# Optimization experiments

Hardware: AMD Instinct MI355X
Metric: run time of the kernel (lower is better)

## Reference

```python
import jax, jax.numpy as jnp
import numpy as np

N = 50000       # nodes
E = 800000      # directed edges (before self-loops)
IN = 128        # in_channels
H = 8           # heads
C = 32          # hidden_channels (per head)
OUT = 4         # out_channels
NS_ATT = 0.2    # PyG GATConv attention leaky-relu slope
NS_ACT = 0.01   # model activation leaky-relu slope
EPS = 1e-5      # BatchNorm eps


def setup_inputs() -> dict:
    key = jax.random.key(0)
    ks = jax.random.split(key, 18)
    s = 0.05
    return {
        "x": jax.random.normal(ks[0], (N, IN), jnp.float32),
        "edge_index": jax.random.randint(ks[1], (2, E), 0, N, dtype=jnp.int32),
        # layer 1: GATConv(IN -> C, heads=H, concat)
        "W1": jax.random.normal(ks[2], (IN, H * C), jnp.float32) * s,
        "as1": jax.random.normal(ks[3], (H, C), jnp.float32) * s,
        "ad1": jax.random.normal(ks[4], (H, C), jnp.float32) * s,
        "b1": jnp.zeros((H * C,), jnp.float32),
        "g1": jnp.ones((H * C,), jnp.float32),
        "be1": jnp.zeros((H * C,), jnp.float32),
        # middle layer: GATConv(H*C -> C, heads=H, concat) + BN + residual
        "W2": jax.random.normal(ks[5], (H * C, H * C), jnp.float32) * s,
        "as2": jax.random.normal(ks[6], (H, C), jnp.float32) * s,
        "ad2": jax.random.normal(ks[7], (H, C), jnp.float32) * s,
        "b2": jnp.zeros((H * C,), jnp.float32),
        "g2": jnp.ones((H * C,), jnp.float32),
        "be2": jnp.zeros((H * C,), jnp.float32),
        # final layer: GATConv(H*C -> OUT, heads=1, concat=False)
        "W3": jax.random.normal(ks[8], (H * C, OUT), jnp.float32) * s,
        "as3": jax.random.normal(ks[9], (1, OUT), jnp.float32) * s,
        "ad3": jax.random.normal(ks[10], (1, OUT), jnp.float32) * s,
        "b3": jnp.zeros((OUT,), jnp.float32),
    }


def _lrelu(x, slope):
    return jnp.where(x >= 0, x, slope * x)


def _gat_conv(x, src, dst, W, a_src, a_dst, bias, heads, ch, concat):
    # PyG GATConv: h = x @ W per head; edge logit = LReLU(a_src.h_j + a_dst.h_i)
    n = x.shape[0]
    h = (x @ W).reshape(n, heads, ch)                      # [N,H,C]
    al_s = jnp.sum(h * a_src, axis=-1)                     # [N,H]
    al_d = jnp.sum(h * a_dst, axis=-1)                     # [N,H]
    logits = _lrelu(al_s[src] + al_d[dst], NS_ATT)         # [E,H]
    # segment softmax over edges grouped by destination node
    m = jax.ops.segment_max(logits, dst, num_segments=n)   # [N,H]
    e = jnp.exp(logits - m[dst])
    denom = jax.ops.segment_sum(e, dst, num_segments=n)
    alpha = e / (denom[dst] + 1e-16)                       # [E,H]
    out = jax.ops.segment_sum(alpha[:, :, None] * h[src], dst, num_segments=n)  # [N,H,C]
    if concat:
        return out.reshape(n, heads * ch) + bias
    return out.mean(axis=1) + bias


def _bn(x, gamma, beta):
    mu = jnp.mean(x, axis=0)
    var = jnp.mean((x - mu) ** 2, axis=0)
    return (x - mu) * jax.lax.rsqrt(var + EPS) * gamma + beta


def reference(x, edge_index, W1, as1, ad1, b1, g1, be1,
              W2, as2, ad2, b2, g2, be2, W3, as3, ad3, b3):
    n = x.shape[0]
    loops = jnp.arange(n, dtype=edge_index.dtype)          # self-loops (PyG default)
    src = jnp.concatenate([edge_index[0], loops])
    dst = jnp.concatenate([edge_index[1], loops])
    h = _lrelu(_bn(_gat_conv(x, src, dst, W1, as1, ad1, b1, H, C, True), g1, be1), NS_ACT)
    residual = h
    h = _lrelu(_bn(_gat_conv(h, src, dst, W2, as2, ad2, b2, H, C, True), g2, be2), NS_ACT)
    h = h + residual
    return _gat_conv(h, src, dst, W3, as3, ad3, b3, 1, OUT, False)
```

## Files before the change

kernel.cpp:

```cpp
#include <hip/hip_runtime.h>

typedef __attribute__((ext_vector_type(8))) short bf16x8;
typedef __attribute__((ext_vector_type(4))) float f32x4;

__device__ __forceinline__ float lrelu(float x, float s) { return x >= 0.f ? x : s * x; }
__device__ __forceinline__ float b2f(unsigned short u) {
  union { unsigned int i; float f; } v; v.i = ((unsigned int)u) << 16; return v.f;
}
__device__ __forceinline__ float b2f_lo(unsigned int u) {
  union { unsigned int i; float f; } v; v.i = u << 16; return v.f;
}
__device__ __forceinline__ float b2f_hi(unsigned int u) {
  union { unsigned int i; float f; } v; v.i = u & 0xffff0000u; return v.f;
}
__device__ __forceinline__ unsigned short f2b(float f) {
  union { float f; unsigned int i; } v; v.f = f;
  unsigned int r = v.i + 0x7fffu + ((v.i >> 16) & 1u);
  return (unsigned short)(r >> 16);
}
__device__ __forceinline__ unsigned int fbits(float f) {
  union { float f; unsigned int i; } v; v.f = f; return v.i;
}
__device__ __forceinline__ float bitsf(unsigned int u) {
  union { unsigned int i; float f; } v; v.i = u; return v.f;
}

__global__ __launch_bounds__(256) void k_hist(const int* __restrict__ dst, int e,
                                              int* __restrict__ cnt) {
  int i = blockIdx.x * 256 + threadIdx.x;
  if (i < e) atomicAdd(&cnt[dst[i]], 1);
}

__global__ __launch_bounds__(256) void k_bsum(const int* __restrict__ cnt,
                                              int* __restrict__ bsum, int n) {
  const int base = blockIdx.x * 1024;
  const int t = threadIdx.x;
  int s = 0;
#pragma unroll
  for (int i = 0; i < 4; ++i) {
    int idx = base + t + i * 256;
    if (idx < n) s += cnt[idx] + 1;
  }
#pragma unroll
  for (int off = 1; off < 64; off <<= 1) s += __shfl_xor(s, off);
  __shared__ int ws[4];
  const int lane = t & 63, w = t >> 6;
  if (lane == 0) ws[w] = s;
  __syncthreads();
  if (t == 0) bsum[blockIdx.x] = ws[0] + ws[1] + ws[2] + ws[3];
}

__global__ __launch_bounds__(64) void k_scanb(const int* __restrict__ bsum,
                                              int* __restrict__ boff,
                                              int* __restrict__ ptrN, int B) {
  const int lane = threadIdx.x;
  int v = lane < B ? bsum[lane] : 0;
  int incl = v;
#pragma unroll
  for (int off = 1; off < 64; off <<= 1) {
    int u = __shfl_up(incl, off);
    if (lane >= off) incl += u;
  }
  if (lane < B) boff[lane] = incl - v;
  if (lane == 63) *ptrN = incl;
}

__global__ __launch_bounds__(256) void k_scanl(const int* __restrict__ cnt,
                                               const int* __restrict__ boff,
                                               int* __restrict__ ptr,
                                               int* __restrict__ fill, int n) {
  __shared__ int ws[4];
  const int t = threadIdx.x;
  const int base = blockIdx.x * 1024 + t * 4;
  int v0 = base + 0 < n ? cnt[base + 0] + 1 : 0;
  int v1 = base + 1 < n ? cnt[base + 1] + 1 : 0;
  int v2 = base + 2 < n ? cnt[base + 2] + 1 : 0;
  int v3 = base + 3 < n ? cnt[base + 3] + 1 : 0;
  const int tsum = v0 + v1 + v2 + v3;
  const int lane = t & 63, w = t >> 6;
  int incl = tsum;
#pragma unroll
  for (int off = 1; off < 64; off <<= 1) {
    int u = __shfl_up(incl, off);
    if (lane >= off) incl += u;
  }
  if (lane == 63) ws[w] = incl;
  __syncthreads();
  int excl = boff[blockIdx.x] + incl - tsum;
  for (int i = 0; i < w; ++i) excl += ws[i];
  if (base + 0 < n) { ptr[base + 0] = excl; fill[base + 0] = excl; }
  excl += v0;
  if (base + 1 < n) { ptr[base + 1] = excl; fill[base + 1] = excl; }
  excl += v1;
  if (base + 2 < n) { ptr[base + 2] = excl; fill[base + 2] = excl; }
  excl += v2;
  if (base + 3 < n) { ptr[base + 3] = excl; fill[base + 3] = excl; }
}

__global__ __launch_bounds__(256) void k_scatter(const int* __restrict__ srce,
                                                 const int* __restrict__ dste,
                                                 int e, int n,
                                                 int* __restrict__ fill,
                                                 int* __restrict__ srcs) {
  int i = blockIdx.x * 256 + threadIdx.x;
  if (i < e) {
    int pos = atomicAdd(&fill[dste[i]], 1);
    srcs[pos] = srce[i];
  } else if (i < e + n) {
    int v = i - e;
    int pos = atomicAdd(&fill[v], 1);
    srcs[pos] = v;
  }
}

__global__ __launch_bounds__(256) void k_prep(const float* __restrict__ x,
                                              unsigned short* __restrict__ xb,
                                              const float* __restrict__ W1,
                                              unsigned short* __restrict__ w1t,
                                              const float* __restrict__ W2,
                                              unsigned short* __restrict__ w2t, int n4) {
  int i = blockIdx.x * 256 + threadIdx.x;
  if (i < n4) {
    float4 v = ((const float4*)x)[i];
    ushort4 o;
    o.x = f2b(v.x); o.y = f2b(v.y); o.z = f2b(v.z); o.w = f2b(v.w);
    ((ushort4*)xb)[i] = o;
    return;
  }
  i -= n4;
  if (i < 256 * 128) {
    int nn = i / 128, k = i - nn * 128;
    w1t[i] = f2b(W1[(size_t)k * 256 + nn]);
    return;
  }
  i -= 256 * 128;
  if (i < 256 * 256) {
    int nn = i / 256, k = i - nn * 256;
    w2t[i] = f2b(W2[(size_t)k * 256 + nn]);
  }
}

__global__ __launch_bounds__(256) void k_mfma(const unsigned short* __restrict__ A,
                                              const unsigned short* __restrict__ BT,
                                              unsigned short* __restrict__ C,
                                              const float* __restrict__ as_,
                                              const float* __restrict__ ad_,
                                              float* __restrict__ als,
                                              float* __restrict__ ald,
                                              int M, int Nn, int K) {
  __shared__ unsigned int Asu[128 * 20];
  __shared__ unsigned int Bsu[128 * 20];
  const int tid = threadIdx.x;
  const int bm = blockIdx.x * 128, bn = blockIdx.y * 128;
  const int w = tid >> 6, lane = tid & 63;
  const int wm = w >> 1, wn = w & 1;
  const int l16 = lane & 15, lg = lane >> 4;
  f32x4 acc[4][4] = {};
  for (int k0 = 0; k0 < K; k0 += 32) {
#pragma unroll
    for (int rep = 0; rep < 2; ++rep) {
      int ci = tid + rep * 256;
      int row = ci >> 2, cg = ci & 3;
      int ar = bm + row;
      ar = ar < M ? ar : M - 1;
      uint4 av = *(const uint4*)(A + (size_t)ar * K + k0 + cg * 8);
      *(uint4*)&Asu[row * 20 + cg * 4] = av;
      uint4 bv = *(const uint4*)(BT + (size_t)(bn + row) * K + k0 + cg * 8);
      *(uint4*)&Bsu[row * 20 + cg * 4] = bv;
    }
    __syncthreads();
    bf16x8 aF[4], bF[4];
#pragma unroll
    for (int mi = 0; mi < 4; ++mi)
      aF[mi] = *(const bf16x8*)&Asu[(wm * 64 + mi * 16 + l16) * 20 + lg * 4];
#pragma unroll
    for (int ni = 0; ni < 4; ++ni)
      bF[ni] = *(const bf16x8*)&Bsu[(wn * 64 + ni * 16 + l16) * 20 + lg * 4];
#pragma unroll
    for (int mi = 0; mi < 4; ++mi)
#pragma unroll
      for (int ni = 0; ni < 4; ++ni)
        acc[mi][ni] =
            __builtin_amdgcn_mfma_f32_16x16x32_bf16(aF[mi], bF[ni], acc[mi][ni], 0, 0, 0);
    __syncthreads();
  }
  float asv[4], adv[4];
#pragma unroll
  for (int ni = 0; ni < 4; ++ni) {
    int gcol = bn + wn * 64 + ni * 16 + l16;
    asv[ni] = as_[gcol];
    adv[ni] = ad_[gcol];
  }
  const int hb = (bn >> 5) + wn * 2;
#pragma unroll
  for (int mi = 0; mi < 4; ++mi) {
#pragma unroll
    for (int r = 0; r < 4; ++r) {
      int grow = bm + wm * 64 + mi * 16 + lg * 4 + r;
      bool ok = grow < M;
      if (ok) {
#pragma unroll
        for (int ni = 0; ni < 4; ++ni) {
          int gcol = bn + wn * 64 + ni * 16 + l16;
          C[(size_t)grow * Nn + gcol] = f2b(acc[mi][ni][r]);
        }
      }
      float ps0 = acc[mi][0][r] * asv[0] + acc[mi][1][r] * asv[1];
      float ps1 = acc[mi][2][r] * asv[2] + acc[mi][3][r] * asv[3];
      float pd0 = acc[mi][0][r] * adv[0] + acc[mi][1][r] * adv[1];
      float pd1 = acc[mi][2][r] * adv[2] + acc[mi][3][r] * adv[3];
#pragma unroll
      for (int off = 1; off < 16; off <<= 1) {
        ps0 += __shfl_xor(ps0, off);
        ps1 += __shfl_xor(ps1, off);
        pd0 += __shfl_xor(pd0, off);
        pd1 += __shfl_xor(pd1, off);
      }
      if (ok && l16 == 0) {
        *(float2*)(als + (size_t)grow * 8 + hb) = make_float2(ps0, ps1);
        *(float2*)(ald + (size_t)grow * 8 + hb) = make_float2(pd0, pd1);
      }
    }
  }
}

__global__ __launch_bounds__(256) void k_agg(const unsigned short* __restrict__ h,
                                             const float* __restrict__ als,
                                             const float* __restrict__ ald,
                                             const int* __restrict__ ptr,
                                             const int* __restrict__ srcs,
                                             const float* __restrict__ bias,
                                             unsigned short* __restrict__ out, int n) {
  int wid = (blockIdx.x * 256 + threadIdx.x) >> 6;
  int lane = threadIdx.x & 63;
  if (wid >= n) return;
  const int beg = ptr[wid], end = ptr[wid + 1];
  const int L = lane & 15;
  const int e = lane >> 4;
  const int hh = L >> 1;
  const float adh = ald[(size_t)wid * 8 + hh];
  float s = 0.f;
  float a0 = 0, a1 = 0, a2 = 0, a3 = 0, a4 = 0, a5 = 0, a6 = 0, a7 = 0;
  float a8 = 0, a9 = 0, aA = 0, aB = 0, aC = 0, aD = 0, aE = 0, aF = 0;
  int j = beg + e;
  int s0 = j < end ? srcs[j] : 0;
  int s1 = (j + 4) < end ? srcs[j + 4] : 0;
  const uint4* hp0 = (const uint4*)(h + (size_t)s0 * 256 + L * 16);
  uint4 c0 = hp0[0];
  uint4 c1 = hp0[1];
  float alsc = als[(size_t)s0 * 8 + hh];
  for (; j < end; j += 4) {
    int s2 = (j + 8) < end ? srcs[j + 8] : 0;
    const uint4* hp1 = (const uint4*)(h + (size_t)s1 * 256 + L * 16);
    uint4 n0 = hp1[0];
    uint4 n1 = hp1[1];
    float alsn = als[(size_t)s1 * 8 + hh];
    float lg = lrelu(alsc + adh, 0.2f);
    float wt = __expf(lg);
    s += wt;
    a0 += wt * b2f_lo(c0.x); a1 += wt * b2f_hi(c0.x);
    a2 += wt * b2f_lo(c0.y); a3 += wt * b2f_hi(c0.y);
    a4 += wt * b2f_lo(c0.z); a5 += wt * b2f_hi(c0.z);
    a6 += wt * b2f_lo(c0.w); a7 += wt * b2f_hi(c0.w);
    a8 += wt * b2f_lo(c1.x); a9 += wt * b2f_hi(c1.x);
    aA += wt * b2f_lo(c1.y); aB += wt * b2f_hi(c1.y);
    aC += wt * b2f_lo(c1.z); aD += wt * b2f_hi(c1.z);
    aE += wt * b2f_lo(c1.w); aF += wt * b2f_hi(c1.w);
    c0 = n0; c1 = n1; alsc = alsn;
    s1 = s2;
  }
  a0 += __shfl_xor(a0, 16); a0 += __shfl_xor(a0, 32);
  a1 += __shfl_xor(a1, 16); a1 += __shfl_xor(a1, 32);
  a2 += __shfl_xor(a2, 16); a2 += __shfl_xor(a2, 32);
  a3 += __shfl_xor(a3, 16); a3 += __shfl_xor(a3, 32);
  a4 += __shfl_xor(a4, 16); a4 += __shfl_xor(a4, 32);
  a5 += __shfl_xor(a5, 16); a5 += __shfl_xor(a5, 32);
  a6 += __shfl_xor(a6, 16); a6 += __shfl_xor(a6, 32);
  a7 += __shfl_xor(a7, 16); a7 += __shfl_xor(a7, 32);
  a8 += __shfl_xor(a8, 16); a8 += __shfl_xor(a8, 32);
  a9 += __shfl_xor(a9, 16); a9 += __shfl_xor(a9, 32);
  aA += __shfl_xor(aA, 16); aA += __shfl_xor(aA, 32);
  aB += __shfl_xor(aB, 16); aB += __shfl_xor(aB, 32);
  aC += __shfl_xor(aC, 16); aC += __shfl_xor(aC, 32);
  aD += __shfl_xor(aD, 16); aD += __shfl_xor(aD, 32);
  aE += __shfl_xor(aE, 16); aE += __shfl_xor(aE, 32);
  aF += __shfl_xor(aF, 16); aF += __shfl_xor(aF, 32);
  s += __shfl_xor(s, 16); s += __shfl_xor(s, 32);
  const float inv = 1.f / (s + 1e-16f);
  if (e == 0) {
    const float4* bp = (const float4*)(bias + L * 16);
    float4 b0 = bp[0], b1 = bp[1], b2 = bp[2], b3 = bp[3];
    uint4 o0, o1;
    o0.x = (unsigned int)f2b(a0 * inv + b0.x) | ((unsigned int)f2b(a1 * inv + b0.y) << 16);
    o0.y = (unsigned int)f2b(a2 * inv + b0.z) | ((unsigned int)f2b(a3 * inv + b0.w) << 16);
    o0.z = (unsigned int)f2b(a4 * inv + b1.x) | ((unsigned int)f2b(a5 * inv + b1.y) << 16);
    o0.w = (unsigned int)f2b(a6 * inv + b1.z) | ((unsigned int)f2b(a7 * inv + b1.w) << 16);
    o1.x = (unsigned int)f2b(a8 * inv + b2.x) | ((unsigned int)f2b(a9 * inv + b2.y) << 16);
    o1.y = (unsigned int)f2b(aA * inv + b2.z) | ((unsigned int)f2b(aB * inv + b2.w) << 16);
    o1.z = (unsigned int)f2b(aC * inv + b3.x) | ((unsigned int)f2b(aD * inv + b3.y) << 16);
    o1.w = (unsigned int)f2b(aE * inv + b3.z) | ((unsigned int)f2b(aF * inv + b3.w) << 16);
    uint4* op = (uint4*)(out + (size_t)wid * 256 + L * 16);
    op[0] = o0;
    op[1] = o1;
  }
}

__global__ __launch_bounds__(256) void k_bnp1(const unsigned short* __restrict__ x,
                                              float* __restrict__ partial, int n) {
  const int t = threadIdx.x;
  const int q = t & 63;
  const int rsub = t >> 6;
  float s0 = 0, s1 = 0, s2 = 0, s3 = 0, q0 = 0, q1 = 0, q2 = 0, q3 = 0;
  int r = blockIdx.x * 4 + rsub;
  for (; r + 6144 < n; r += 8192) {
    ushort4 va = *(const ushort4*)(x + (size_t)r * 256 + q * 4);
    ushort4 vb = *(const ushort4*)(x + (size_t)(r + 2048) * 256 + q * 4);
    ushort4 vc = *(const ushort4*)(x + (size_t)(r + 4096) * 256 + q * 4);
    ushort4 vd = *(const ushort4*)(x + (size_t)(r + 6144) * 256 + q * 4);
    float f;
    f = b2f(va.x); s0 += f; q0 += f * f;
    f = b2f(va.y); s1 += f; q1 += f * f;
    f = b2f(va.z); s2 += f; q2 += f * f;
    f = b2f(va.w); s3 += f; q3 += f * f;
    f = b2f(vb.x); s0 += f; q0 += f * f;
    f = b2f(vb.y); s1 += f; q1 += f * f;
    f = b2f(vb.z); s2 += f; q2 += f * f;
    f = b2f(vb.w); s3 += f; q3 += f * f;
    f = b2f(vc.x); s0 += f; q0 += f * f;
    f = b2f(vc.y); s1 += f; q1 += f * f;
    f = b2f(vc.z); s2 += f; q2 += f * f;
    f = b2f(vc.w); s3 += f; q3 += f * f;
    f = b2f(vd.x); s0 += f; q0 += f * f;
    f = b2f(vd.y); s1 += f; q1 += f * f;
    f = b2f(vd.z); s2 += f; q2 += f * f;
    f = b2f(vd.w); s3 += f; q3 += f * f;
  }
  for (; r < n; r += 2048) {
    ushort4 v = *(const ushort4*)(x + (size_t)r * 256 + q * 4);
    float f;
    f = b2f(v.x); s0 += f; q0 += f * f;
    f = b2f(v.y); s1 += f; q1 += f * f;
    f = b2f(v.z); s2 += f; q2 += f * f;
    f = b2f(v.w); s3 += f; q3 += f * f;
  }
  __shared__ float ls[4][512];
  ls[rsub][q * 4 + 0] = s0; ls[rsub][q * 4 + 1] = s1;
  ls[rsub][q * 4 + 2] = s2; ls[rsub][q * 4 + 3] = s3;
  ls[rsub][256 + q * 4 + 0] = q0; ls[rsub][256 + q * 4 + 1] = q1;
  ls[rsub][256 + q * 4 + 2] = q2; ls[rsub][256 + q * 4 + 3] = q3;
  __syncthreads();
  float a = ls[0][t] + ls[1][t] + ls[2][t] + ls[3][t];
  float b = ls[0][256 + t] + ls[1][256 + t] + ls[2][256 + t] + ls[3][256 + t];
  partial[blockIdx.x * 512 + t] = a;
  partial[blockIdx.x * 512 + 256 + t] = b;
}

__global__ __launch_bounds__(256) void k_bnp2(const float* __restrict__ partial,
                                              const float* __restrict__ ga,
                                              const float* __restrict__ be,
                                              float* __restrict__ ss, float invn) {
  const int c = blockIdx.x * 4 + (threadIdx.x >> 6);
  const int lane = threadIdx.x & 63;
  float s = 0.f, qq = 0.f;
#pragma unroll
  for (int k = 0; k < 8; ++k) {
    int b = lane + k * 64;
    s += partial[(size_t)b * 512 + c];
    qq += partial[(size_t)b * 512 + 256 + c];
  }
#pragma unroll
  for (int off = 1; off < 64; off <<= 1) {
    s += __shfl_xor(s, off);
    qq += __shfl_xor(qq, off);
  }
  if (lane == 0) {
    float mu = s * invn;
    float var = qq * invn - mu * mu;
    float sc = ga[c] * rsqrtf(var + 1e-5f);
    ss[c] = sc;
    ss[256 + c] = be[c] - mu * sc;
  }
}

__global__ __launch_bounds__(256) void k_bnact(const unsigned short* __restrict__ x,
                                               const float* __restrict__ ss,
                                               unsigned short* __restrict__ out, int n) {
  const int tot4 = n * 64;
  for (int t = blockIdx.x * 256 + threadIdx.x; t < tot4; t += gridDim.x * 256) {
    int i0 = t * 4;
    int c = i0 & 255;
    ushort4 xu = *(const ushort4*)(x + i0);
    float4 scv = *(const float4*)(ss + c);
    float4 shv = *(const float4*)(ss + 256 + c);
    float t0 = b2f(xu.x) * scv.x + shv.x;
    float t1 = b2f(xu.y) * scv.y + shv.y;
    float t2 = b2f(xu.z) * scv.z + shv.z;
    float t3 = b2f(xu.w) * scv.w + shv.w;
    float o0 = fmaxf(t0, 0.01f * t0);
    float o1 = fmaxf(t1, 0.01f * t1);
    float o2 = fmaxf(t2, 0.01f * t2);
    float o3 = fmaxf(t3, 0.01f * t3);
    ushort4 ob;
    ob.x = f2b(o0); ob.y = f2b(o1); ob.z = f2b(o2); ob.w = f2b(o3);
    *(ushort4*)(out + i0) = ob;
  }
}

__global__ __launch_bounds__(256) void k_bnact3(const unsigned short* __restrict__ x,
                                                const float* __restrict__ ss,
                                                const unsigned short* __restrict__ res,
                                                const float* __restrict__ W3,
                                                const float* __restrict__ as3,
                                                const float* __restrict__ ad3,
                                                uint4* __restrict__ h3p, int n) {
  int wid = (blockIdx.x * 256 + threadIdx.x) >> 6;
  int lane = threadIdx.x & 63;
  if (wid >= n) return;
  const int c = lane * 4;
  ushort4 xu = *(const ushort4*)(x + (size_t)wid * 256 + c);
  ushort4 rv = *(const ushort4*)(res + (size_t)wid * 256 + c);
  float4 scv = *(const float4*)(ss + c);
  float4 shv = *(const float4*)(ss + 256 + c);
  float t0 = b2f(xu.x) * scv.x + shv.x;
  float t1 = b2f(xu.y) * scv.y + shv.y;
  float t2 = b2f(xu.z) * scv.z + shv.z;
  float t3 = b2f(xu.w) * scv.w + shv.w;
  float o0 = fmaxf(t0, 0.01f * t0) + b2f(rv.x);
  float o1 = fmaxf(t1, 0.01f * t1) + b2f(rv.y);
  float o2 = fmaxf(t2, 0.01f * t2) + b2f(rv.z);
  float o3 = fmaxf(t3, 0.01f * t3) + b2f(rv.w);
  const float4* Wp = (const float4*)W3 + lane * 4;
  float4 w0 = Wp[0], w1 = Wp[1], w2 = Wp[2], w3 = Wp[3];
  float a0 = o0 * w0.x + o1 * w1.x + o2 * w2.x + o3 * w3.x;
  float a1 = o0 * w0.y + o1 * w1.y + o2 * w2.y + o3 * w3.y;
  float a2 = o0 * w0.z + o1 * w1.z + o2 * w2.z + o3 * w3.z;
  float a3 = o0 * w0.w + o1 * w1.w + o2 * w2.w + o3 * w3.w;
#pragma unroll
  for (int off = 1; off < 64; off <<= 1) {
    a0 += __shfl_xor(a0, off);
    a1 += __shfl_xor(a1, off);
    a2 += __shfl_xor(a2, off);
    a3 += __shfl_xor(a3, off);
  }
  if (lane == 0) {
    float als3v = a0 * as3[0] + a1 * as3[1] + a2 * as3[2] + a3 * as3[3];
    float ald3v = a0 * ad3[0] + a1 * ad3[1] + a2 * ad3[2] + a3 * ad3[3];
    uint4 pv;
    pv.x = (unsigned int)f2b(a0) | ((unsigned int)f2b(a1) << 16);
    pv.y = (unsigned int)f2b(a2) | ((unsigned int)f2b(a3) << 16);
    pv.z = fbits(als3v);
    pv.w = fbits(ald3v);
    h3p[wid] = pv;
  }
}

__global__ __launch_bounds__(256) void k_agg3(const uint4* __restrict__ h3p,
                                              const int* __restrict__ ptr,
                                              const int* __restrict__ srcs,
                                              const float* __restrict__ b3,
                                              float* __restrict__ out, int n) {
  int wid = (blockIdx.x * 256 + threadIdx.x) >> 6;
  int lane = threadIdx.x & 63;
  if (wid >= n) return;
  const int beg = ptr[wid], end = ptr[wid + 1];
  const float aldh = bitsf(h3p[wid].w);
  float s = 0.f, a0 = 0.f, a1 = 0.f, a2 = 0.f, a3 = 0.f;
  for (int j = beg + lane; j < end; j += 64) {
    uint4 v = h3p[srcs[j]];
    float wgt = __expf(lrelu(bitsf(v.z) + aldh, 0.2f));
    s += wgt;
    a0 += wgt * b2f_lo(v.x);
    a1 += wgt * b2f_hi(v.x);
    a2 += wgt * b2f_lo(v.y);
    a3 += wgt * b2f_hi(v.y);
  }
#pragma unroll
  for (int off = 1; off < 64; off <<= 1) {
    s += __shfl_xor(s, off);
    a0 += __shfl_xor(a0, off);
    a1 += __shfl_xor(a1, off);
    a2 += __shfl_xor(a2, off);
    a3 += __shfl_xor(a3, off);
  }
  if (lane == 0) {
    float inv = 1.f / (s + 1e-16f);
    out[(size_t)wid * 4 + 0] = a0 * inv + b3[0];
    out[(size_t)wid * 4 + 1] = a1 * inv + b3[1];
    out[(size_t)wid * 4 + 2] = a2 * inv + b3[2];
    out[(size_t)wid * 4 + 3] = a3 * inv + b3[3];
  }
}

extern "C" void kernel_launch(void* const* d_in, const int* in_sizes, int n_in,
                              void* d_out, int out_size, void* d_ws, size_t ws_size,
                              hipStream_t stream) {
  const float* x   = (const float*)d_in[0];
  const int*   ei  = (const int*)d_in[1];
  const float* W1  = (const float*)d_in[2];
  const float* as1 = (const float*)d_in[3];
  const float* ad1 = (const float*)d_in[4];
  const float* b1  = (const float*)d_in[5];
  const float* ga1 = (const float*)d_in[6];
  const float* be1 = (const float*)d_in[7];
  const float* W2  = (const float*)d_in[8];
  const float* as2 = (const float*)d_in[9];
  const float* ad2 = (const float*)d_in[10];
  const float* b2  = (const float*)d_in[11];
  const float* ga2 = (const float*)d_in[12];
  const float* be2 = (const float*)d_in[13];
  const float* W3  = (const float*)d_in[14];
  const float* as3 = (const float*)d_in[15];
  const float* ad3 = (const float*)d_in[16];
  const float* b3  = (const float*)d_in[17];

  const int N = in_sizes[0] / 128;
  const int E = in_sizes[1] / 2;
  const int ET = E + N;
  float* out = (float*)d_out;

  char* w = (char*)d_ws;
  auto alloc = [&](size_t bytes) -> void* {
    void* p = (void*)w;
    w += (bytes + 255) & ~(size_t)255;
    return p;
  };
  int* ptr              = (int*)alloc((size_t)(N + 1) * 4);
  int* fill             = (int*)alloc((size_t)N * 4);
  int* cnt              = (int*)alloc((size_t)N * 4);
  int* bsum             = (int*)alloc(64 * 4);
  int* boff             = (int*)alloc(64 * 4);
  int* srcs             = (int*)alloc((size_t)ET * 4);
  unsigned short* hbuf  = (unsigned short*)alloc((size_t)N * 256 * 2);
  unsigned short* aggb  = (unsigned short*)alloc((size_t)N * 256 * 2);
  unsigned short* a1b   = (unsigned short*)alloc((size_t)N * 256 * 2);
  unsigned short* xb    = (unsigned short*)alloc((size_t)N * 128 * 2);
  unsigned short* w1t   = (unsigned short*)alloc(256 * 128 * 2);
  unsigned short* w2t   = (unsigned short*)alloc(256 * 256 * 2);
  float* als            = (float*)alloc((size_t)N * 8 * 4);
  float* ald            = (float*)alloc((size_t)N * 8 * 4);
  uint4* h3p            = (uint4*)alloc((size_t)N * 16);
  float* partial        = (float*)alloc(512 * 512 * 4);
  float* ss             = (float*)alloc(1024 * 4);

  const int* esrc = ei;
  const int* edst = ei + E;
  const float invn = 1.f / (float)N;

  hipMemsetAsync(cnt, 0, (size_t)N * 4, stream);

  const int B = (N + 1023) / 1024;
  k_hist<<<(E + 255) / 256, 256, 0, stream>>>(edst, E, cnt);
  k_bsum<<<B, 256, 0, stream>>>(cnt, bsum, N);
  k_scanb<<<1, 64, 0, stream>>>(bsum, boff, ptr + N, B);
  k_scanl<<<B, 256, 0, stream>>>(cnt, boff, ptr, fill, N);
  k_scatter<<<(ET + 255) / 256, 256, 0, stream>>>(esrc, edst, E, N, fill, srcs);

  const int n4 = N * 32;
  const int prep_tot = n4 + 256 * 128 + 256 * 256;
  k_prep<<<(prep_tot + 255) / 256, 256, 0, stream>>>(x, xb, W1, w1t, W2, w2t, n4);

  const dim3 gemm_grid((N + 127) / 128, 2);
  const int wblocks = (N + 3) / 4;

  k_mfma<<<gemm_grid, 256, 0, stream>>>(xb, w1t, hbuf, as1, ad1, als, ald, N, 256, 128);
  k_agg<<<wblocks, 256, 0, stream>>>(hbuf, als, ald, ptr, srcs, b1, aggb, N);
  k_bnp1<<<512, 256, 0, stream>>>(aggb, partial, N);
  k_bnp2<<<64, 256, 0, stream>>>(partial, ga1, be1, ss, invn);
  k_bnact<<<2048, 256, 0, stream>>>(aggb, ss, a1b, N);

  k_mfma<<<gemm_grid, 256, 0, stream>>>(a1b, w2t, hbuf, as2, ad2, als, ald, N, 256, 256);
  k_agg<<<wblocks, 256, 0, stream>>>(hbuf, als, ald, ptr, srcs, b2, aggb, N);
  k_bnp1<<<512, 256, 0, stream>>>(aggb, partial, N);
  k_bnp2<<<64, 256, 0, stream>>>(partial, ga2, be2, ss + 512, invn);
  k_bnact3<<<wblocks, 256, 0, stream>>>(aggb, ss + 512, a1b, W3, as3, ad3, h3p, N);

  k_agg3<<<wblocks, 256, 0, stream>>>(h3p, ptr, srcs, b3, out, N);
}
```

Baseline: 376.5 us.

## Trim launches, fold memset into prep, and use 16-lane groups in final aggregation

The separate block-offset scan kernel is removed: each scanl block now scans the block sums itself. The memset of the count array moves into the prep kernel, which now runs first. The final single-head aggregation gives each node 16 lanes instead of a full 64-lane wavefront, with a vectorized float4 output store. The scatter writes use nontemporal stores. Together these cut launch count and idle lanes, at the cost of redundant per-block scans and less parallelism for high-degree nodes.

```diff
diff --git a/kernel.cpp b/kernel.cpp
--- a/kernel.cpp
+++ b/kernel.cpp
@@ -50,27 +50,24 @@
   if (t == 0) bsum[blockIdx.x] = ws[0] + ws[1] + ws[2] + ws[3];
 }
 
-__global__ __launch_bounds__(64) void k_scanb(const int* __restrict__ bsum,
-                                              int* __restrict__ boff,
-                                              int* __restrict__ ptrN, int B) {
-  const int lane = threadIdx.x;
-  int v = lane < B ? bsum[lane] : 0;
-  int incl = v;
-#pragma unroll
-  for (int off = 1; off < 64; off <<= 1) {
-    int u = __shfl_up(incl, off);
-    if (lane >= off) incl += u;
-  }
-  if (lane < B) boff[lane] = incl - v;
-  if (lane == 63) *ptrN = incl;
-}
-
 __global__ __launch_bounds__(256) void k_scanl(const int* __restrict__ cnt,
-                                               const int* __restrict__ boff,
+                                               const int* __restrict__ bsum,
                                                int* __restrict__ ptr,
-                                               int* __restrict__ fill, int n) {
+                                               int* __restrict__ fill, int n, int B) {
   __shared__ int ws[4];
+  __shared__ int bo;
   const int t = threadIdx.x;
+  if (t < 64) {
+    int v = t < B ? bsum[t] : 0;
+    int incl = v;
+#pragma unroll
+    for (int off = 1; off < 64; off <<= 1) {
+      int u = __shfl_up(incl, off);
+      if (t >= off) incl += u;
+    }
+    if (t == blockIdx.x) bo = incl - v;
+    if (blockIdx.x == 0 && t == 63) ptr[n] = incl;
+  }
   const int base = blockIdx.x * 1024 + t * 4;
   int v0 = base + 0 < n ? cnt[base + 0] + 1 : 0;
   int v1 = base + 1 < n ? cnt[base + 1] + 1 : 0;
@@ -86,7 +83,7 @@
   }
   if (lane == 63) ws[w] = incl;
   __syncthreads();
-  int excl = boff[blockIdx.x] + incl - tsum;
+  int excl = bo + incl - tsum;
   for (int i = 0; i < w; ++i) excl += ws[i];
   if (base + 0 < n) { ptr[base + 0] = excl; fill[base + 0] = excl; }
   excl += v0;
@@ -105,21 +102,27 @@
   int i = blockIdx.x * 256 + threadIdx.x;
   if (i < e) {
     int pos = atomicAdd(&fill[dste[i]], 1);
-    srcs[pos] = srce[i];
+    __builtin_nontemporal_store(srce[i], &srcs[pos]);
   } else if (i < e + n) {
     int v = i - e;
     int pos = atomicAdd(&fill[v], 1);
-    srcs[pos] = v;
-  }
-}
-
-__global__ __launch_bounds__(256) void k_prep(const float* __restrict__ x,
+    __builtin_nontemporal_store(v, &srcs[pos]);
+  }
+}
+
+__global__ __launch_bounds__(256) void k_prep(int* __restrict__ cnt, int n,
+                                              const float* __restrict__ x,
                                               unsigned short* __restrict__ xb,
                                               const float* __restrict__ W1,
                                               unsigned short* __restrict__ w1t,
                                               const float* __restrict__ W2,
                                               unsigned short* __restrict__ w2t, int n4) {
   int i = blockIdx.x * 256 + threadIdx.x;
+  if (i < n) {
+    cnt[i] = 0;
+    return;
+  }
+  i -= n;
   if (i < n4) {
     float4 v = ((const float4*)x)[i];
     ushort4 o;
@@ -129,13 +132,13 @@
   }
   i -= n4;
   if (i < 256 * 128) {
-    int nn = i / 128, k = i - nn * 128;
+    int nn = i >> 7, k = i & 127;
     w1t[i] = f2b(W1[(size_t)k * 256 + nn]);
     return;
   }
   i -= 256 * 128;
   if (i < 256 * 256) {
-    int nn = i / 256, k = i - nn * 256;
+    int nn = i >> 8, k = i & 255;
     w2t[i] = f2b(W2[(size_t)k * 256 + nn]);
   }
 }
@@ -459,13 +462,20 @@
                                               const int* __restrict__ srcs,
                                               const float* __restrict__ b3,
                                               float* __restrict__ out, int n) {
-  int wid = (blockIdx.x * 256 + threadIdx.x) >> 6;
-  int lane = threadIdx.x & 63;
-  if (wid >= n) return;
-  const int beg = ptr[wid], end = ptr[wid + 1];
-  const float aldh = bitsf(h3p[wid].w);
+  const int wv = (blockIdx.x * 256 + threadIdx.x) >> 6;
+  const int lane = threadIdx.x & 63;
+  const int sl = lane & 15;
+  const int node = wv * 4 + (lane >> 4);
+  const bool ok = node < n;
+  int beg = 0, end = 0;
+  float aldh = 0.f;
+  if (ok) {
+    beg = ptr[node];
+    end = ptr[node + 1];
+    aldh = bitsf(h3p[node].w);
+  }
   float s = 0.f, a0 = 0.f, a1 = 0.f, a2 = 0.f, a3 = 0.f;
-  for (int j = beg + lane; j < end; j += 64) {
+  for (int j = beg + sl; j < end; j += 16) {
     uint4 v = h3p[srcs[j]];
     float wgt = __expf(lrelu(bitsf(v.z) + aldh, 0.2f));
     s += wgt;
@@ -475,19 +485,21 @@
     a3 += wgt * b2f_hi(v.y);
   }
 #pragma unroll
-  for (int off = 1; off < 64; off <<= 1) {
+  for (int off = 1; off < 16; off <<= 1) {
     s += __shfl_xor(s, off);
     a0 += __shfl_xor(a0, off);
     a1 += __shfl_xor(a1, off);
     a2 += __shfl_xor(a2, off);
     a3 += __shfl_xor(a3, off);
   }
-  if (lane == 0) {
+  if (ok && sl == 0) {
     float inv = 1.f / (s + 1e-16f);
-    out[(size_t)wid * 4 + 0] = a0 * inv + b3[0];
-    out[(size_t)wid * 4 + 1] = a1 * inv + b3[1];
-    out[(size_t)wid * 4 + 2] = a2 * inv + b3[2];
-    out[(size_t)wid * 4 + 3] = a3 * inv + b3[3];
+    float4 o;
+    o.x = a0 * inv + b3[0];
+    o.y = a1 * inv + b3[1];
+    o.z = a2 * inv + b3[2];
+    o.w = a3 * inv + b3[3];
+    *(float4*)(out + (size_t)node * 4) = o;
   }
 }
 
@@ -528,7 +540,6 @@
   int* fill             = (int*)alloc((size_t)N * 4);
   int* cnt              = (int*)alloc((size_t)N * 4);
   int* bsum             = (int*)alloc(64 * 4);
-  int* boff             = (int*)alloc(64 * 4);
   int* srcs             = (int*)alloc((size_t)ET * 4);
   unsigned short* hbuf  = (unsigned short*)alloc((size_t)N * 256 * 2);
   unsigned short* aggb  = (unsigned short*)alloc((size_t)N * 256 * 2);
@@ -546,21 +557,19 @@
   const int* edst = ei + E;
   const float invn = 1.f / (float)N;
 
-  hipMemsetAsync(cnt, 0, (size_t)N * 4, stream);
+  const int n4 = N * 32;
+  const int prep_tot = N + n4 + 256 * 128 + 256 * 256;
+  k_prep<<<(prep_tot + 255) / 256, 256, 0, stream>>>(cnt, N, x, xb, W1, w1t, W2, w2t, n4);
 
   const int B = (N + 1023) / 1024;
   k_hist<<<(E + 255) / 256, 256, 0, stream>>>(edst, E, cnt);
   k_bsum<<<B, 256, 0, stream>>>(cnt, bsum, N);
-  k_scanb<<<1, 64, 0, stream>>>(bsum, boff, ptr + N, B);
-  k_scanl<<<B, 256, 0, stream>>>(cnt, boff, ptr, fill, N);
+  k_scanl<<<B, 256, 0, stream>>>(cnt, bsum, ptr, fill, N, B);
   k_scatter<<<(ET + 255) / 256, 256, 0, stream>>>(esrc, edst, E, N, fill, srcs);
-
-  const int n4 = N * 32;
-  const int prep_tot = n4 + 256 * 128 + 256 * 256;
-  k_prep<<<(prep_tot + 255) / 256, 256, 0, stream>>>(x, xb, W1, w1t, W2, w2t, n4);
 
   const dim3 gemm_grid((N + 127) / 128, 2);
   const int wblocks = (N + 3) / 4;
+  const int wblocks4 = (N + 15) / 16;
 
   k_mfma<<<gemm_grid, 256, 0, stream>>>(xb, w1t, hbuf, as1, ad1, als, ald, N, 256, 128);
   k_agg<<<wblocks, 256, 0, stream>>>(hbuf, als, ald, ptr, srcs, b1, aggb, N);
@@ -574,5 +583,5 @@
   k_bnp2<<<64, 256, 0, stream>>>(partial, ga2, be2, ss + 512, invn);
   k_bnact3<<<wblocks, 256, 0, stream>>>(aggb, ss + 512, a1b, W3, as3, ad3, h3p, N);
 
-  k_agg3<<<wblocks, 256, 0, stream>>>(h3p, ptr, srcs, b3, out, N);
-}
+  k_agg3<<<wblocks4, 256, 0, stream>>>(h3p, ptr, srcs, b3, out, N);
+}
```

New measurement: 365.1 us. 1.03x faster.
